# Optimization experiments

Hardware: AMD Instinct MI355X
Metric: run time of the kernel (lower is better)

## Reference

```python
import jax, jax.numpy as jnp
import numpy as np

B, Q, K, HID, NH = 32, 300, 2048, 256, 8
HD = HID // NH  # 32; expanded head dim = 64

def _lin_params(key, out_f, in_f):
    kw, kb = jax.random.split(key)
    w = jax.random.normal(kw, (out_f, in_f), jnp.float32) * (1.0 / np.sqrt(in_f))
    b = jax.random.normal(kb, (out_f,), jnp.float32) * 0.01
    return w, b

def setup_inputs() -> dict:
    key = jax.random.key(0)
    ks = jax.random.split(key, 12)
    inp = {
        'hidden_states': jax.random.normal(ks[0], (B, Q, HID), jnp.float32),
        'encoder_hidden_states': jax.random.normal(ks[1], (B, K, HID), jnp.float32),
        'query_sine_embed': jax.random.normal(ks[2], (B, Q, HID), jnp.float32),
        'encoder_position_embeddings': jax.random.normal(ks[3], (B, K, HID), jnp.float32),
        'query_position_embeddings': jax.random.normal(ks[4], (B, Q, HID), jnp.float32),
    }
    names = ['qc', 'qp', 'kc', 'kp', 'v', 'qs', 'o']
    for i, n in enumerate(names):
        w, b = _lin_params(ks[5 + i], HID, HID)
        inp[n + '_w'] = w
        inp[n + '_b'] = b
    return inp

def _lin(x, w, b):
    return x @ w.T + b

def reference(hidden_states, encoder_hidden_states, query_sine_embed,
              encoder_position_embeddings, query_position_embeddings,
              qc_w, qc_b, qp_w, qp_b, kc_w, kc_b, kp_w, kp_b,
              v_w, v_b, qs_w, qs_b, o_w, o_b):
    b, q, _ = hidden_states.shape
    k = encoder_hidden_states.shape[1]
    # content / position projections
    q_c = _lin(hidden_states, qc_w, qc_b)
    k_c = _lin(encoder_hidden_states, kc_w, kc_b)
    v = _lin(encoder_hidden_states, v_w, v_b)
    k_pos = _lin(encoder_position_embeddings, kp_w, kp_b)
    # first-layer branch: query_position_embeddings provided
    q_c = q_c + _lin(query_position_embeddings, qp_w, qp_b)
    k_c = k_c + k_pos
    # split heads and concat sine/pos embeddings along head dim (doubling it)
    q_c = q_c.reshape(b, q, NH, HD)
    q_s = _lin(query_sine_embed, qs_w, qs_b).reshape(b, q, NH, HD)
    k_c = k_c.reshape(b, k, NH, HD)
    k_p = k_pos.reshape(b, k, NH, HD)
    q_full = jnp.concatenate([q_c, q_s], axis=-1)   # [B,Q,NH,2*HD]
    k_full = jnp.concatenate([k_c, k_p], axis=-1)   # [B,K,NH,2*HD]
    v = v.reshape(b, k, NH, HD)
    scaling = (2 * HD) ** -0.5
    # eager attention
    scores = jnp.einsum('bqhd,bkhd->bhqk', q_full, k_full) * scaling
    attn_weights = jax.nn.softmax(scores, axis=-1)  # [B,NH,Q,K]
    attn_out = jnp.einsum('bhqk,bkhd->bqhd', attn_weights, v)
    attn_out = attn_out.reshape(b, q, HID)
    attn_out = _lin(attn_out, o_w, o_b)
    return attn_out, attn_weights
```

## Files before the change

### kernel.cpp

```cpp
#include <hip/hip_runtime.h>
#include <hip/hip_bf16.h>

typedef __hip_bfloat16 bf16;
typedef __attribute__((ext_vector_type(8))) __bf16 bf16x8;
typedef __attribute__((ext_vector_type(4))) float f32x4;

#define NB 32
#define NQ 300
#define NK 2048
#define NH 8

#define MFMA(a, b, c) __builtin_amdgcn_mfma_f32_16x16x32_bf16(a, b, c, 0, 0, 0)

__device__ __forceinline__ bf16x8 cvt8(float4 a, float4 b) {
    bf16x8 r;
    r[0] = (__bf16)a.x; r[1] = (__bf16)a.y; r[2] = (__bf16)a.z; r[3] = (__bf16)a.w;
    r[4] = (__bf16)b.x; r[5] = (__bf16)b.y; r[6] = (__bf16)b.z; r[7] = (__bf16)b.w;
    return r;
}
__device__ __forceinline__ bf16x8 loadA_f32(const float* p) {
    return cvt8(*(const float4*)p, *(const float4*)(p + 4));
}
__device__ __forceinline__ unsigned pkbf(float a, float b) {
    union { __bf16 h; unsigned short u; } ua, ub;
    ua.h = (__bf16)a; ub.h = (__bf16)b;
    return (unsigned)ua.u | ((unsigned)ub.u << 16);
}

__global__ __launch_bounds__(256) void wprep_kernel(
    const float* __restrict__ w0, const float* __restrict__ w1,
    const float* __restrict__ w2, const float* __restrict__ w3,
    const float* __restrict__ w4, const float* __restrict__ w5,
    const float* __restrict__ w6, bf16* __restrict__ wbf)
{
    const float* Ws[7] = {w0, w1, w2, w3, w4, w5, w6};
    size_t e = ((size_t)blockIdx.x * 256 + threadIdx.x) * 8;
    const float* src = Ws[e >> 16] + (e & 65535);
    bf16x8 v = loadA_f32(src);
    *(bf16x8*)(wbf + e) = v;
}

__global__ __launch_bounds__(128) void qproj_kernel(
    const float* __restrict__ XH, const float* __restrict__ XP,
    const float* __restrict__ XS,
    const bf16* __restrict__ WC, const bf16* __restrict__ WP,
    const bf16* __restrict__ WS,
    const float* __restrict__ bc, const float* __restrict__ bp,
    const float* __restrict__ bs, bf16* __restrict__ q_full)
{
    const int t = threadIdx.x, w = t >> 6, l = t & 63, g = l >> 4, c16 = l & 15;
    const int rbase = blockIdx.x * 32 + w * 16;
    const int row = rbase + c16;

    bf16x8 ah[8], ap[8], as_[8];
    #pragma unroll
    for (int ks = 0; ks < 8; ++ks) {
        ah[ks]  = loadA_f32(XH + (size_t)row * 256 + ks * 32 + g * 8);
        ap[ks]  = loadA_f32(XP + (size_t)row * 256 + ks * 32 + g * 8);
        as_[ks] = loadA_f32(XS + (size_t)row * 256 + ks * 32 + g * 8);
    }
    for (int nt = 0; nt < 16; ++nt) {
        const int n = nt * 16 + c16;
        f32x4 accc = {0.f, 0.f, 0.f, 0.f}, accs = {0.f, 0.f, 0.f, 0.f};
        #pragma unroll
        for (int ks = 0; ks < 8; ++ks) {
            bf16x8 bwc = *(const bf16x8*)(WC + (size_t)n * 256 + ks * 32 + g * 8);
            bf16x8 bwp = *(const bf16x8*)(WP + (size_t)n * 256 + ks * 32 + g * 8);
            bf16x8 bws = *(const bf16x8*)(WS + (size_t)n * 256 + ks * 32 + g * 8);
            accc = MFMA(ah[ks], bwc, accc);
            accc = MFMA(ap[ks], bwp, accc);
            accs = MFMA(as_[ks], bws, accs);
        }
        const float bic = bc[n] + bp[n], bis = bs[n];
        const int h = n >> 5, d = n & 31;
        #pragma unroll
        for (int i = 0; i < 4; ++i) {
            const int r = rbase + 4 * g + i;
            const int b_ = (int)(((unsigned)r * 55925u) >> 24);
            const int q = r - b_ * 300;
            const size_t base = (((size_t)b_ * 8 + h) * NQ + q) * 64;
            q_full[base + d]      = __float2bfloat16((accc[i] + bic) * 0.125f);
            q_full[base + 32 + d] = __float2bfloat16((accs[i] + bis) * 0.125f);
        }
    }
}

__global__ __launch_bounds__(256) void kvproj_kernel(
    const float* __restrict__ X1, const float* __restrict__ X2,
    const bf16* __restrict__ W1, const bf16* __restrict__ W2,
    const bf16* __restrict__ WV,
    const float* __restrict__ b1, const float* __restrict__ b2,
    const float* __restrict__ bvb,
    bf16* __restrict__ k_full, bf16* __restrict__ v_t)
{
    const int t = threadIdx.x, w = t >> 6, l = t & 63, g = l >> 4, c16 = l & 15;
    const int wm = w >> 1, wn = w & 1;
    const int r0 = blockIdx.x * 64 + wm * 32;

    bf16x8 a1[2][8], a2[2][8];
    #pragma unroll
    for (int mt = 0; mt < 2; ++mt) {
        const int row = r0 + mt * 16 + c16;
        #pragma unroll
        for (int ks = 0; ks < 8; ++ks) {
            a1[mt][ks] = loadA_f32(X1 + (size_t)row * 256 + ks * 32 + g * 8);
            a2[mt][ks] = loadA_f32(X2 + (size_t)row * 256 + ks * 32 + g * 8);
        }
    }
    #pragma unroll
    for (int nt = 0; nt < 8; ++nt) {
        const int n  = wn * 128 + nt * 16 + c16;
        const int n0 = wn * 128 + nt * 16 + 4 * g;
        f32x4 tc0 = {0.f,0.f,0.f,0.f}, tc1 = {0.f,0.f,0.f,0.f};
        f32x4 tp0 = {0.f,0.f,0.f,0.f}, tp1 = {0.f,0.f,0.f,0.f};
        f32x4 av0 = {0.f,0.f,0.f,0.f}, av1 = {0.f,0.f,0.f,0.f};
        #pragma unroll
        for (int ks = 0; ks < 8; ++ks) {
            bf16x8 bw1 = *(const bf16x8*)(W1 + (size_t)n * 256 + ks * 32 + g * 8);
            bf16x8 bw2 = *(const bf16x8*)(W2 + (size_t)n * 256 + ks * 32 + g * 8);
            bf16x8 bwv = *(const bf16x8*)(WV + (size_t)n * 256 + ks * 32 + g * 8);
            tc0 = MFMA(bw1, a1[0][ks], tc0);
            tp0 = MFMA(bw2, a2[0][ks], tp0);
            av0 = MFMA(a1[0][ks], bwv, av0);
            tc1 = MFMA(bw1, a1[1][ks], tc1);
            tp1 = MFMA(bw2, a2[1][ks], tp1);
            av1 = MFMA(a1[1][ks], bwv, av1);
        }
        const f32x4 bc4 = *(const f32x4*)(b1 + n0);
        const f32x4 bp4 = *(const f32x4*)(b2 + n0);
        const float bvn = bvb[n];
        const int h0 = n0 >> 5, d0 = n0 & 31;
        const int hv = n >> 5,  dv = n & 31;
        #pragma unroll
        for (int mt = 0; mt < 2; ++mt) {
            f32x4 tc = mt ? tc1 : tc0;
            f32x4 tp = mt ? tp1 : tp0;
            const int kq = r0 + mt * 16 + c16;
            const int bk = kq >> 11, kkq = kq & 2047;
            const size_t kb = ((size_t)(bk * 8 + h0) * NK + kkq) * 64;
            const float y0 = tp[0] + bp4[0], y1 = tp[1] + bp4[1];
            const float y2 = tp[2] + bp4[2], y3 = tp[3] + bp4[3];
            uint2 kc2 = { pkbf(tc[0] + bc4[0] + y0, tc[1] + bc4[1] + y1),
                          pkbf(tc[2] + bc4[2] + y2, tc[3] + bc4[3] + y3) };
            uint2 kp2 = { pkbf(y0, y1), pkbf(y2, y3) };
            *(uint2*)&k_full[kb + d0]      = kc2;
            *(uint2*)&k_full[kb + 32 + d0] = kp2;
            f32x4 av = mt ? av1 : av0;
            const int rr = r0 + mt * 16 + 4 * g;
            const int bv = rr >> 11, kkv = rr & 2047;
            uint2 vpk = { pkbf(av[0] + bvn, av[1] + bvn),
                          pkbf(av[2] + bvn, av[3] + bvn) };
            *(uint2*)&v_t[((size_t)(bv * 8 + hv) * 32 + dv) * NK + kkv] = vpk;
        }
    }
}

__global__ __launch_bounds__(256) void attn1_kernel(
    const bf16* __restrict__ q_full, const bf16* __restrict__ k_full,
    float* __restrict__ inv_arr)
{
    __shared__ float psum[4][64];

    const int t = threadIdx.x, w = t >> 6, l = t & 63;
    const int g = l >> 4, c16 = l & 15;

    const int p = blockIdx.x;
    const int lid = (p & 7) * 160 + (p >> 3);
    const int bh = (int)(((unsigned)lid * 6554u) >> 15);
    const int blk = lid - bh * 5;

    const size_t qbase = (size_t)bh * NQ * 64;
    const size_t kbase = (size_t)bh * NK * 64;

    bf16x8 qt0[4], qt1[4];
    #pragma unroll
    for (int qt = 0; qt < 4; ++qt) {
        const int qr = min(blk * 64 + qt * 16 + c16, NQ - 1);
        qt0[qt] = *(const bf16x8*)(q_full + qbase + (size_t)qr * 64 + g * 8);
        qt1[qt] = *(const bf16x8*)(q_full + qbase + (size_t)qr * 64 + 32 + g * 8);
    }
    float sums[4] = {0.f, 0.f, 0.f, 0.f};
    const int kw0 = w * 512;
    for (int ch = 0; ch < 32; ++ch) {
        const bf16* kap = k_full + kbase + (size_t)(kw0 + ch * 16 + c16) * 64 + g * 8;
        bf16x8 ka0 = *(const bf16x8*)(kap);
        bf16x8 ka1 = *(const bf16x8*)(kap + 32);
        #pragma unroll
        for (int qt = 0; qt < 4; ++qt) {
            f32x4 sa = {0.f, 0.f, 0.f, 0.f};
            sa = MFMA(ka0, qt0[qt], sa);
            sa = MFMA(ka1, qt1[qt], sa);
            sums[qt] += __expf(sa[0]) + __expf(sa[1])
                      + __expf(sa[2]) + __expf(sa[3]);
        }
    }
    #pragma unroll
    for (int qt = 0; qt < 4; ++qt) {
        sums[qt] += __shfl_xor(sums[qt], 16);
        sums[qt] += __shfl_xor(sums[qt], 32);
    }
    if (l < 16) {
        #pragma unroll
        for (int qt = 0; qt < 4; ++qt) psum[w][qt * 16 + l] = sums[qt];
    }
    __syncthreads();

    if (t < 64) {
        const int q = blk * 64 + t;
        if (q < NQ)
            inv_arr[(size_t)bh * NQ + q] =
                1.f / (psum[0][t] + psum[1][t] + psum[2][t] + psum[3][t]);
    }
}

__global__ __launch_bounds__(256) void attn2_kernel(
    const bf16* __restrict__ q_full, const bf16* __restrict__ k_full,
    const bf16* __restrict__ v_t, const float* __restrict__ inv_arr,
    float* __restrict__ w_out, float* __restrict__ attn_tmp)
{
    __shared__ __align__(16) unsigned smem[8192];

    const int t = threadIdx.x, w = t >> 6, l = t & 63;
    const int g = l >> 4, c16 = l & 15;
    const int s4 = (c16 & 3) << 2;

    const int p = blockIdx.x;
    const int lid = (p & 7) * 160 + (p >> 3);
    const int bh = (int)(((unsigned)lid * 6554u) >> 15);
    const int blk = lid - bh * 5;
    const int q0b = blk * 64;

    const size_t qbase = (size_t)bh * NQ * 64;
    const size_t kbase = (size_t)bh * NK * 64;
    const size_t vbase = (size_t)bh * 32 * NK;

    bf16x8 qf0[4], qf1[4];
    float invt[4];
    float* wrow[4];
    bool qok[4];
    #pragma unroll
    for (int qt = 0; qt < 4; ++qt) {
        const int qq = q0b + qt * 16 + c16;
        const int qr = min(qq, NQ - 1);
        qf0[qt] = *(const bf16x8*)(q_full + qbase + (size_t)qr * 64 + g * 8);
        qf1[qt] = *(const bf16x8*)(q_full + qbase + (size_t)qr * 64 + 32 + g * 8);
        invt[qt] = inv_arr[(size_t)bh * NQ + qr];
        wrow[qt] = w_out + ((size_t)bh * NQ + qr) * NK;
        qok[qt] = qq < NQ;
    }

    const int kw0 = w * 512;
    const bf16* kbp = k_full + kbase;
    const bf16* vbp = v_t + vbase;
    unsigned* pawW = smem + w * 2048;

    f32x4 oa0[4], oa1[4];
    #pragma unroll
    for (int qt = 0; qt < 4; ++qt) {
        oa0[qt] = (f32x4){0.f, 0.f, 0.f, 0.f};
        oa1[qt] = (f32x4){0.f, 0.f, 0.f, 0.f};
    }

#define LDK(c, K00, K01, K10, K11) do { \
    const bf16* _kap = kbp + (size_t)(kw0 + (c) * 32 + c16) * 64 + g * 8; \
    K00 = *(const bf16x8*)(_kap); \
    K01 = *(const bf16x8*)(_kap + 32); \
    K10 = *(const bf16x8*)(_kap + 16 * 64); \
    K11 = *(const bf16x8*)(_kap + 16 * 64 + 32); \
} while (0)
#define LDV(c, V0, V1) do { \
    const bf16* _vp = vbp + (size_t)c16 * NK + kw0 + (c) * 32 + g * 8; \
    V0 = *(const bf16x8*)(_vp); \
    V1 = *(const bf16x8*)(_vp + 16 * NK); \
} while (0)

#define BODY(c, PAR, K00, K01, K10, K11, V0, V1) do { \
    const int _k0 = kw0 + (c) * 32; \
    const int _cn = ((c) + 2 < 16) ? (c) + 2 : (c); \
    unsigned* _paw = pawW + (PAR) * 1024; \
    _Pragma("unroll") \
    for (int _qt = 0; _qt < 4; ++_qt) { \
        f32x4 _slo = {0.f,0.f,0.f,0.f}, _shi = {0.f,0.f,0.f,0.f}; \
        _slo = MFMA(K00, qf0[_qt], _slo); _slo = MFMA(K01, qf1[_qt], _slo); \
        _shi = MFMA(K10, qf0[_qt], _shi); _shi = MFMA(K11, qf1[_qt], _shi); \
        if (_qt == 3) LDK(_cn, K00, K01, K10, K11);    \
        float _plo[4], _phi[4]; \
        _Pragma("unroll") \
        for (int _i = 0; _i < 4; ++_i) { \
            _plo[_i] = __expf(_slo[_i]) * invt[_qt]; \
            _phi[_i] = __expf(_shi[_i]) * invt[_qt]; \
        } \
        if (qok[_qt]) { \
            f32x4 _vlo = {_plo[0], _plo[1], _plo[2], _plo[3]}; \
            f32x4 _vhi = {_phi[0], _phi[1], _phi[2], _phi[3]}; \
            __builtin_nontemporal_store(_vlo, (f32x4*)(wrow[_qt] + _k0 + 4 * g)); \
            __builtin_nontemporal_store(_vhi, (f32x4*)(wrow[_qt] + _k0 + 16 + 4 * g)); \
        } \
        unsigned* _pq = _paw + _qt * 256; \
        uint2 _lo2 = { pkbf(_plo[0], _plo[1]), pkbf(_plo[2], _plo[3]) }; \
        uint2 _hi2 = { pkbf(_phi[0], _phi[1]), pkbf(_phi[2], _phi[3]) }; \
        *(uint2*)&_pq[c16 * 16 + ((2 * g) ^ s4)]     = _lo2; \
        *(uint2*)&_pq[c16 * 16 + ((8 + 2 * g) ^ s4)] = _hi2; \
        union { uint4 q; bf16x8 v; } _A; \
        _A.q = *(uint4*)&_pq[c16 * 16 + ((4 * g) ^ s4)]; \
        oa0[_qt] = MFMA(_A.v, V0, oa0[_qt]); \
        oa1[_qt] = MFMA(_A.v, V1, oa1[_qt]); \
        if (_qt == 3) LDV(_cn, V0, V1);                \
    } \
} while (0)

    bf16x8 Ak00, Ak01, Ak10, Ak11, Av0, Av1;
    bf16x8 Bk00, Bk01, Bk10, Bk11, Bv0, Bv1;
    LDK(0, Ak00, Ak01, Ak10, Ak11);  LDV(0, Av0, Av1);
    LDK(1, Bk00, Bk01, Bk10, Bk11);  LDV(1, Bv0, Bv1);

    for (int c = 0; c < 16; c += 2) {
        BODY(c,     0, Ak00, Ak01, Ak10, Ak11, Av0, Av1);
        BODY(c + 1, 1, Bk00, Bk01, Bk10, Bk11, Bv0, Bv1);
    }
#undef BODY
#undef LDV
#undef LDK

    float* redw = (float*)smem + w * 2048;
    #pragma unroll
    for (int qt = 0; qt < 4; ++qt) {
        #pragma unroll
        for (int i = 0; i < 4; ++i) {
            const int q = qt * 16 + 4 * g + i;
            redw[q * 32 + c16]      = oa0[qt][i];
            redw[q * 32 + 16 + c16] = oa1[qt][i];
        }
    }
    __syncthreads();

    const float* redf = (const float*)smem;
    const int b_ = bh >> 3, h = bh & 7;
    #pragma unroll
    for (int i = 0; i < 8; ++i) {
        const int idx = t + 256 * i;
        const int q = idx >> 5, d = idx & 31;
        if (q0b + q < NQ)
            attn_tmp[((size_t)b_ * NQ + q0b + q) * 256 + h * 32 + d] =
                redf[0 * 2048 + q * 32 + d] + redf[1 * 2048 + q * 32 + d] +
                redf[2 * 2048 + q * 32 + d] + redf[3 * 2048 + q * 32 + d];
    }
}

__global__ __launch_bounds__(256) void oproj_kernel(
    const float* __restrict__ X1, const bf16* __restrict__ W1,
    const float* __restrict__ b1, float* __restrict__ out)
{
    const int t = threadIdx.x, w = t >> 6, l = t & 63, g = l >> 4, c16 = l & 15;
    const int wm = w >> 1, wn = w & 1;
    const int r0 = blockIdx.x * 64 + wm * 32;

    bf16x8 a1[2][8];
    #pragma unroll
    for (int mt = 0; mt < 2; ++mt) {
        const int row = r0 + mt * 16 + c16;
        #pragma unroll
        for (int ks = 0; ks < 8; ++ks)
            a1[mt][ks] = loadA_f32(X1 + (size_t)row * 256 + ks * 32 + g * 8);
    }
    #pragma unroll
    for (int nt = 0; nt < 8; ++nt) {
        const int n = wn * 128 + nt * 16 + c16;
        f32x4 acc0 = {0.f,0.f,0.f,0.f}, acc1 = {0.f,0.f,0.f,0.f};
        #pragma unroll
        for (int ks = 0; ks < 8; ++ks) {
            bf16x8 bw1 = *(const bf16x8*)(W1 + (size_t)n * 256 + ks * 32 + g * 8);
            acc0 = MFMA(a1[0][ks], bw1, acc0);
            acc1 = MFMA(a1[1][ks], bw1, acc1);
        }
        const float bias = b1[n];
        #pragma unroll
        for (int mt = 0; mt < 2; ++mt) {
            f32x4 acc = mt ? acc1 : acc0;
            #pragma unroll
            for (int i = 0; i < 4; ++i) {
                const int r = r0 + mt * 16 + 4 * g + i;
                out[(size_t)r * 256 + n] = acc[i] + bias;
            }
        }
    }
}

extern "C" void kernel_launch(void* const* d_in, const int* in_sizes, int n_in,
                              void* d_out, int out_size, void* d_ws, size_t ws_size,
                              hipStream_t stream) {
    const float* hidden = (const float*)d_in[0];
    const float* enc    = (const float*)d_in[1];
    const float* sine   = (const float*)d_in[2];
    const float* encpos = (const float*)d_in[3];
    const float* qpos   = (const float*)d_in[4];
    const float* qc_w = (const float*)d_in[5];  const float* qc_b = (const float*)d_in[6];
    const float* qp_w = (const float*)d_in[7];  const float* qp_b = (const float*)d_in[8];
    const float* kc_w = (const float*)d_in[9];  const float* kc_b = (const float*)d_in[10];
    const float* kp_w = (const float*)d_in[11]; const float* kp_b = (const float*)d_in[12];
    const float* v_w  = (const float*)d_in[13]; const float* v_b  = (const float*)d_in[14];
    const float* qs_w = (const float*)d_in[15]; const float* qs_b = (const float*)d_in[16];
    const float* o_w  = (const float*)d_in[17]; const float* o_b  = (const float*)d_in[18];

    float* out = (float*)d_out;
    float* attn_out = out;
    float* w_out    = out + (size_t)NB * NQ * 256;

    char* ws = (char*)d_ws;
    bf16* q_full    = (bf16*)ws;
    bf16* k_full    = (bf16*)(ws + 9830400);
    bf16* v_t       = (bf16*)(ws + 76939264);
    float* attn_tmp = (float*)(ws + 110493696);
    bf16* wbf       = (bf16*)(ws + 120324096);
    float* inv_arr  = (float*)(ws + 121241600);

    wprep_kernel<<<224, 256, 0, stream>>>(qc_w, qp_w, kc_w, kp_w, v_w, qs_w, o_w, wbf);

    qproj_kernel<<<300, 128, 0, stream>>>(hidden, qpos, sine,
        wbf + 0 * 65536, wbf + 1 * 65536, wbf + 5 * 65536,
        qc_b, qp_b, qs_b, q_full);
    kvproj_kernel<<<1024, 256, 0, stream>>>(enc, encpos,
        wbf + 2 * 65536, wbf + 3 * 65536, wbf + 4 * 65536,
        kc_b, kp_b, v_b, k_full, v_t);

    attn1_kernel<<<1280, 256, 0, stream>>>(q_full, k_full, inv_arr);
    attn2_kernel<<<1280, 256, 0, stream>>>(q_full, k_full, v_t, inv_arr, w_out, attn_tmp);

    oproj_kernel<<<150, 256, 0, stream>>>(attn_tmp, wbf + 6 * 65536, o_b, attn_out);
}
```

Baseline: 466.0 us.

## Fuse softmax-denominator pass into attention kernel to avoid second launch

```diff
diff --git a/kernel.cpp b/kernel.cpp
--- a/kernel.cpp
+++ b/kernel.cpp
@@ -155,69 +155,12 @@
     }
 }
 
-__global__ __launch_bounds__(256) void attn1_kernel(
+__global__ __launch_bounds__(256) void attn_kernel(
     const bf16* __restrict__ q_full, const bf16* __restrict__ k_full,
-    float* __restrict__ inv_arr)
+    const bf16* __restrict__ v_t, float* __restrict__ w_out,
+    float* __restrict__ attn_tmp)
 {
     __shared__ float psum[4][64];
-
-    const int t = threadIdx.x, w = t >> 6, l = t & 63;
-    const int g = l >> 4, c16 = l & 15;
-
-    const int p = blockIdx.x;
-    const int lid = (p & 7) * 160 + (p >> 3);
-    const int bh = (int)(((unsigned)lid * 6554u) >> 15);
-    const int blk = lid - bh * 5;
-
-    const size_t qbase = (size_t)bh * NQ * 64;
-    const size_t kbase = (size_t)bh * NK * 64;
-
-    bf16x8 qt0[4], qt1[4];
-    #pragma unroll
-    for (int qt = 0; qt < 4; ++qt) {
-        const int qr = min(blk * 64 + qt * 16 + c16, NQ - 1);
-        qt0[qt] = *(const bf16x8*)(q_full + qbase + (size_t)qr * 64 + g * 8);
-        qt1[qt] = *(const bf16x8*)(q_full + qbase + (size_t)qr * 64 + 32 + g * 8);
-    }
-    float sums[4] = {0.f, 0.f, 0.f, 0.f};
-    const int kw0 = w * 512;
-    for (int ch = 0; ch < 32; ++ch) {
-        const bf16* kap = k_full + kbase + (size_t)(kw0 + ch * 16 + c16) * 64 + g * 8;
-        bf16x8 ka0 = *(const bf16x8*)(kap);
-        bf16x8 ka1 = *(const bf16x8*)(kap + 32);
-        #pragma unroll
-        for (int qt = 0; qt < 4; ++qt) {
-            f32x4 sa = {0.f, 0.f, 0.f, 0.f};
-            sa = MFMA(ka0, qt0[qt], sa);
-            sa = MFMA(ka1, qt1[qt], sa);
-            sums[qt] += __expf(sa[0]) + __expf(sa[1])
-                      + __expf(sa[2]) + __expf(sa[3]);
-        }
-    }
-    #pragma unroll
-    for (int qt = 0; qt < 4; ++qt) {
-        sums[qt] += __shfl_xor(sums[qt], 16);
-        sums[qt] += __shfl_xor(sums[qt], 32);
-    }
-    if (l < 16) {
-        #pragma unroll
-        for (int qt = 0; qt < 4; ++qt) psum[w][qt * 16 + l] = sums[qt];
-    }
-    __syncthreads();
-
-    if (t < 64) {
-        const int q = blk * 64 + t;
-        if (q < NQ)
-            inv_arr[(size_t)bh * NQ + q] =
-                1.f / (psum[0][t] + psum[1][t] + psum[2][t] + psum[3][t]);
-    }
-}
-
-__global__ __launch_bounds__(256) void attn2_kernel(
-    const bf16* __restrict__ q_full, const bf16* __restrict__ k_full,
-    const bf16* __restrict__ v_t, const float* __restrict__ inv_arr,
-    float* __restrict__ w_out, float* __restrict__ attn_tmp)
-{
     __shared__ __align__(16) unsigned smem[8192];
 
     const int t = threadIdx.x, w = t >> 6, l = t & 63;
@@ -235,7 +178,6 @@
     const size_t vbase = (size_t)bh * 32 * NK;
 
     bf16x8 qf0[4], qf1[4];
-    float invt[4];
     float* wrow[4];
     bool qok[4];
     #pragma unroll
@@ -244,7 +186,6 @@
         const int qr = min(qq, NQ - 1);
         qf0[qt] = *(const bf16x8*)(q_full + qbase + (size_t)qr * 64 + g * 8);
         qf1[qt] = *(const bf16x8*)(q_full + qbase + (size_t)qr * 64 + 32 + g * 8);
-        invt[qt] = inv_arr[(size_t)bh * NQ + qr];
         wrow[qt] = w_out + ((size_t)bh * NQ + qr) * NK;
         qok[qt] = qq < NQ;
     }
@@ -253,13 +194,6 @@
     const bf16* kbp = k_full + kbase;
     const bf16* vbp = v_t + vbase;
     unsigned* pawW = smem + w * 2048;
-
-    f32x4 oa0[4], oa1[4];
-    #pragma unroll
-    for (int qt = 0; qt < 4; ++qt) {
-        oa0[qt] = (f32x4){0.f, 0.f, 0.f, 0.f};
-        oa1[qt] = (f32x4){0.f, 0.f, 0.f, 0.f};
-    }
 
 #define LDK(c, K00, K01, K10, K11) do { \
     const bf16* _kap = kbp + (size_t)(kw0 + (c) * 32 + c16) * 64 + g * 8; \
@@ -274,6 +208,60 @@
     V1 = *(const bf16x8*)(_vp + 16 * NK); \
 } while (0)
 
+    float sums[4] = {0.f, 0.f, 0.f, 0.f};
+
+#define SBODY(c, K00, K01, K10, K11) do { \
+    const int _cn = ((c) + 2 < 16) ? (c) + 2 : (c); \
+    _Pragma("unroll") \
+    for (int _qt = 0; _qt < 4; ++_qt) { \
+        f32x4 _slo = {0.f,0.f,0.f,0.f}, _shi = {0.f,0.f,0.f,0.f}; \
+        _slo = MFMA(K00, qf0[_qt], _slo); _slo = MFMA(K01, qf1[_qt], _slo); \
+        _shi = MFMA(K10, qf0[_qt], _shi); _shi = MFMA(K11, qf1[_qt], _shi); \
+        if (_qt == 3) LDK(_cn, K00, K01, K10, K11); \
+        sums[_qt] += __expf(_slo[0]) + __expf(_slo[1]) \
+                   + __expf(_slo[2]) + __expf(_slo[3]) \
+                   + __expf(_shi[0]) + __expf(_shi[1]) \
+                   + __expf(_shi[2]) + __expf(_shi[3]); \
+    } \
+} while (0)
+
+    {
+        bf16x8 Ak00, Ak01, Ak10, Ak11;
+        bf16x8 Bk00, Bk01, Bk10, Bk11;
+        LDK(0, Ak00, Ak01, Ak10, Ak11);
+        LDK(1, Bk00, Bk01, Bk10, Bk11);
+        for (int c = 0; c < 16; c += 2) {
+            SBODY(c,     Ak00, Ak01, Ak10, Ak11);
+            SBODY(c + 1, Bk00, Bk01, Bk10, Bk11);
+        }
+    }
+#undef SBODY
+
+    #pragma unroll
+    for (int qt = 0; qt < 4; ++qt) {
+        sums[qt] += __shfl_xor(sums[qt], 16);
+        sums[qt] += __shfl_xor(sums[qt], 32);
+    }
+    if (l < 16) {
+        #pragma unroll
+        for (int qt = 0; qt < 4; ++qt) psum[w][qt * 16 + l] = sums[qt];
+    }
+    __syncthreads();
+
+    float invt[4];
+    #pragma unroll
+    for (int qt = 0; qt < 4; ++qt) {
+        const int qi = qt * 16 + c16;
+        invt[qt] = 1.f / (psum[0][qi] + psum[1][qi] + psum[2][qi] + psum[3][qi]);
+    }
+
+    f32x4 oa0[4], oa1[4];
+    #pragma unroll
+    for (int qt = 0; qt < 4; ++qt) {
+        oa0[qt] = (f32x4){0.f, 0.f, 0.f, 0.f};
+        oa1[qt] = (f32x4){0.f, 0.f, 0.f, 0.f};
+    }
+
 #define BODY(c, PAR, K00, K01, K10, K11, V0, V1) do { \
     const int _k0 = kw0 + (c) * 32; \
     const int _cn = ((c) + 2 < 16) ? (c) + 2 : (c); \
@@ -283,7 +271,7 @@
         f32x4 _slo = {0.f,0.f,0.f,0.f}, _shi = {0.f,0.f,0.f,0.f}; \
         _slo = MFMA(K00, qf0[_qt], _slo); _slo = MFMA(K01, qf1[_qt], _slo); \
         _shi = MFMA(K10, qf0[_qt], _shi); _shi = MFMA(K11, qf1[_qt], _shi); \
-        if (_qt == 3) LDK(_cn, K00, K01, K10, K11);    \
+        if (_qt == 3) LDK(_cn, K00, K01, K10, K11); \
         float _plo[4], _phi[4]; \
         _Pragma("unroll") \
         for (int _i = 0; _i < 4; ++_i) { \
@@ -305,18 +293,20 @@
         _A.q = *(uint4*)&_pq[c16 * 16 + ((4 * g) ^ s4)]; \
         oa0[_qt] = MFMA(_A.v, V0, oa0[_qt]); \
         oa1[_qt] = MFMA(_A.v, V1, oa1[_qt]); \
-        if (_qt == 3) LDV(_cn, V0, V1);                \
+        if (_qt == 3) LDV(_cn, V0, V1); \
     } \
 } while (0)
 
-    bf16x8 Ak00, Ak01, Ak10, Ak11, Av0, Av1;
-    bf16x8 Bk00, Bk01, Bk10, Bk11, Bv0, Bv1;
-    LDK(0, Ak00, Ak01, Ak10, Ak11);  LDV(0, Av0, Av1);
-    LDK(1, Bk00, Bk01, Bk10, Bk11);  LDV(1, Bv0, Bv1);
-
-    for (int c = 0; c < 16; c += 2) {
-        BODY(c,     0, Ak00, Ak01, Ak10, Ak11, Av0, Av1);
-        BODY(c + 1, 1, Bk00, Bk01, Bk10, Bk11, Bv0, Bv1);
+    {
+        bf16x8 Ak00, Ak01, Ak10, Ak11, Av0, Av1;
+        bf16x8 Bk00, Bk01, Bk10, Bk11, Bv0, Bv1;
+        LDK(0, Ak00, Ak01, Ak10, Ak11);  LDV(0, Av0, Av1);
+        LDK(1, Bk00, Bk01, Bk10, Bk11);  LDV(1, Bv0, Bv1);
+
+        for (int c = 0; c < 16; c += 2) {
+            BODY(c,     0, Ak00, Ak01, Ak10, Ak11, Av0, Av1);
+            BODY(c + 1, 1, Bk00, Bk01, Bk10, Bk11, Bv0, Bv1);
+        }
     }
 #undef BODY
 #undef LDV
@@ -412,7 +402,6 @@
     bf16* v_t       = (bf16*)(ws + 76939264);
     float* attn_tmp = (float*)(ws + 110493696);
     bf16* wbf       = (bf16*)(ws + 120324096);
-    float* inv_arr  = (float*)(ws + 121241600);
 
     wprep_kernel<<<224, 256, 0, stream>>>(qc_w, qp_w, kc_w, kp_w, v_w, qs_w, o_w, wbf);
 
@@ -423,8 +412,7 @@
         wbf + 2 * 65536, wbf + 3 * 65536, wbf + 4 * 65536,
         kc_b, kp_b, v_b, k_full, v_t);
 
-    attn1_kernel<<<1280, 256, 0, stream>>>(q_full, k_full, inv_arr);
-    attn2_kernel<<<1280, 256, 0, stream>>>(q_full, k_full, v_t, inv_arr, w_out, attn_tmp);
+    attn_kernel<<<1280, 256, 0, stream>>>(q_full, k_full, v_t, w_out, attn_tmp);
 
     oproj_kernel<<<150, 256, 0, stream>>>(attn_tmp, wbf + 6 * 65536, o_b, attn_out);
 }
```

Result: faster. 424.1 us (-9.0%).
